# Kernel tuning notes

Measured on AMD Instinct MI355X. Metric: run time of the kernel, lower is better.

Reference implementation:

```python
import jax, jax.numpy as jnp
import numpy as np

DIM_MODEL = 1024
NUM_HEADS = 16
DIM_HEAD = 64
B, S = 2, 2048


def setup_inputs() -> dict:
    key = jax.random.key(0)
    ks = jax.random.split(key, 10)
    scale = 1.0 / np.sqrt(DIM_MODEL)
    inp = {
        "x": jax.random.normal(ks[0], (B, S, DIM_MODEL), dtype=jnp.float32),
        "padding_mask": jax.random.randint(ks[1], (B, S), 0, 2, dtype=jnp.int32),
        "Wq": jax.random.normal(ks[2], (DIM_MODEL, DIM_MODEL), dtype=jnp.float32) * scale,
        "bq": jnp.zeros((DIM_MODEL,), dtype=jnp.float32),
        "Wk": jax.random.normal(ks[3], (DIM_MODEL, DIM_MODEL), dtype=jnp.float32) * scale,
        "bk": jnp.zeros((DIM_MODEL,), dtype=jnp.float32),
        "Wv": jax.random.normal(ks[4], (DIM_MODEL, DIM_MODEL), dtype=jnp.float32) * scale,
        "bv": jnp.zeros((DIM_MODEL,), dtype=jnp.float32),
        "Wo": jax.random.normal(ks[5], (DIM_MODEL, DIM_MODEL), dtype=jnp.float32) * scale,
        "bo": jnp.zeros((DIM_MODEL,), dtype=jnp.float32),
    }
    return inp


def reference(x, padding_mask, Wq, bq, Wk, bk, Wv, bv, Wo, bo):
    b, s, _ = x.shape
    dot_scale = jnp.sqrt(jnp.asarray(DIM_HEAD, dtype=x.dtype))
    # projections -> (b, h, s, d)
    q = (x @ Wq + bq).reshape(b, s, NUM_HEADS, DIM_HEAD).transpose(0, 2, 1, 3)
    k = (x @ Wk + bk).reshape(b, s, NUM_HEADS, DIM_HEAD).transpose(0, 2, 1, 3)
    v = (x @ Wv + bv).reshape(b, s, NUM_HEADS, DIM_HEAD).transpose(0, 2, 1, 3)
    # scores (b, h, s, s)
    scores = jnp.einsum("bhqd,bhkd->bhqk", q, k) / dot_scale
    mask = (padding_mask == 1)[:, None, None, :]  # (b,1,1,s) over key positions
    scores = jnp.where(mask, -jnp.inf, scores)
    attn = jax.nn.softmax(scores, axis=-1)
    out = jnp.einsum("bhqk,bhkd->bhqd", attn, v)
    out = out.transpose(0, 2, 1, 3).reshape(b, s, NUM_HEADS * DIM_HEAD)
    return out @ Wo + bo
```

## Files before the change

### kernel.cpp

```cpp
#include <hip/hip_runtime.h>
#include <hip/hip_bf16.h>
#include <stdint.h>
#include <math.h>

#define D_MODEL 1024
#define NHEAD   16
#define DHEAD   64
#define BATCH   2
#define SEQ     2048
#define M_TOK   (BATCH * SEQ)

#define QSCALE 0.18033688011112042f

typedef __attribute__((ext_vector_type(8))) short   short8;
typedef __attribute__((ext_vector_type(8))) __bf16  bf16x8;
typedef __attribute__((ext_vector_type(4))) float   f32x4;

__device__ inline short f2bf(float f) {
  unsigned int u = __builtin_bit_cast(unsigned int, f);
  unsigned int r = (u + 0x7FFFu + ((u >> 16) & 1u)) >> 16;
  return (short)(unsigned short)r;
}
__device__ inline short f2bf_fast(float f) {
  unsigned int u = __builtin_bit_cast(unsigned int, f);
  return (short)(unsigned short)((u + 0x8000u) >> 16);
}

__device__ inline void gl_lds16(const void* g, void* l) {
  __builtin_amdgcn_global_load_lds((__attribute__((address_space(1))) void*)(g),
                                   (__attribute__((address_space(3))) void*)(l),
                                   16, 0, 0);
}

__device__ inline bf16x8 lds_frag(const short* p) {
  return *(const bf16x8*)(p);
}
__device__ inline bf16x8 lds_frag64(const short* p) {
  union { bf16x8 v; short4 h[2]; } u;
  u.h[0] = *(const short4*)(p);
  u.h[1] = *(const short4*)(p + 4);
  return u.v;
}

__global__ __launch_bounds__(256) void cvt_bf16(const float* __restrict__ in,
                                                short* __restrict__ out, int n4) {
  int i = blockIdx.x * 256 + threadIdx.x;
  if (i >= n4) return;
  f32x4 v = *(const f32x4*)(in + (size_t)i * 4);
  short4 o;
  o.x = f2bf(v[0]); o.y = f2bf(v[1]); o.z = f2bf(v[2]); o.w = f2bf(v[3]);
  *(short4*)(out + (size_t)i * 4) = o;
}

__global__ __launch_bounds__(256) void transpose_w(const float* __restrict__ w0,
                                                   const float* __restrict__ w1,
                                                   const float* __restrict__ w2,
                                                   const float* __restrict__ w3,
                                                   short* __restrict__ out) {
  __shared__ short tile[64][72];
  const float* W = blockIdx.z == 0 ? w0 : blockIdx.z == 1 ? w1 : blockIdx.z == 2 ? w2 : w3;
  short* O = out + (size_t)blockIdx.z * (D_MODEL * (size_t)D_MODEL);
  int n0 = blockIdx.x * 64, k0 = blockIdx.y * 64;
  int t = threadIdx.x;
#pragma unroll
  for (int i = 0; i < 16; ++i) {
    int idx = t + 256 * i;
    int r = idx >> 6, c = idx & 63;
    tile[r][c] = f2bf(W[(size_t)(k0 + r) * D_MODEL + n0 + c]);
  }
  __syncthreads();
#pragma unroll
  for (int i = 0; i < 16; ++i) {
    int idx = t + 256 * i;
    int r = idx >> 6, c = idx & 63;
    O[(size_t)(n0 + r) * D_MODEL + k0 + c] = tile[c][r];
  }
}

template <bool OUTF32, bool VT>
__global__ __launch_bounds__(256) void gemm128(const short* __restrict__ A,
                                               const short* __restrict__ Bt_base,
                                               const float* __restrict__ b0,
                                               const float* __restrict__ b1,
                                               const float* __restrict__ b2,
                                               void* __restrict__ out_base,
                                               short* __restrict__ vt,
                                               const int* __restrict__ pm) {
  const int z = blockIdx.z;
  const short* Bt   = Bt_base + (size_t)z * (D_MODEL * (size_t)D_MODEL);
  const float* bias = (z == 0) ? b0 : (z == 1) ? b1 : b2;

  __shared__ short As[128 * 64];
  __shared__ short Bs[128 * 64];

  const int t = threadIdx.x;
  const int lane = t & 63;
  const int wid = t >> 6;
  const int wm = (wid >> 1) * 64, wn = (wid & 1) * 64;
  const int m0 = blockIdx.x * 128, n0 = blockIdx.y * 128;
  const int cl = lane & 15, q = lane >> 4;
  const int sw = cl & 7;

  f32x4 acc[4][4];
#pragma unroll
  for (int i = 0; i < 4; ++i)
#pragma unroll
    for (int j = 0; j < 4; ++j) acc[i][j] = 0.0f;

  for (int k0 = 0; k0 < D_MODEL; k0 += 64) {
    __syncthreads();
#pragma unroll
    for (int i = 0; i < 4; ++i) {
      int c = t + 256 * i;
      int row = c >> 3;
      int cp  = c & 7;
      int col = ((cp ^ (row & 7)) * 8);
      gl_lds16(A  + (size_t)(m0 + row) * D_MODEL + k0 + col, (void*)(As + c * 8));
      gl_lds16(Bt + (size_t)(n0 + row) * D_MODEL + k0 + col, (void*)(Bs + c * 8));
    }
    __syncthreads();

    bf16x8 af[4][2], bfr[4][2];
#pragma unroll
    for (int mi = 0; mi < 4; ++mi) {
      af[mi][0] = lds_frag(As + (wm + mi * 16 + cl) * 64 + (q ^ sw) * 8);
      af[mi][1] = lds_frag(As + (wm + mi * 16 + cl) * 64 + ((4 + q) ^ sw) * 8);
    }
#pragma unroll
    for (int ni = 0; ni < 4; ++ni) {
      bfr[ni][0] = lds_frag(Bs + (wn + ni * 16 + cl) * 64 + (q ^ sw) * 8);
      bfr[ni][1] = lds_frag(Bs + (wn + ni * 16 + cl) * 64 + ((4 + q) ^ sw) * 8);
    }
#pragma unroll
    for (int mi = 0; mi < 4; ++mi)
#pragma unroll
      for (int ni = 0; ni < 4; ++ni) {
        acc[mi][ni] = __builtin_amdgcn_mfma_f32_16x16x32_bf16(af[mi][0], bfr[ni][0], acc[mi][ni], 0, 0, 0);
        acc[mi][ni] = __builtin_amdgcn_mfma_f32_16x16x32_bf16(af[mi][1], bfr[ni][1], acc[mi][ni], 0, 0, 0);
      }
  }

  const float oscale = (VT && z == 0) ? QSCALE : 1.0f;
  int4 mm[4];
  if (VT && z == 2) {
#pragma unroll
    for (int mi = 0; mi < 4; ++mi) {
      int rbase = m0 + wm + mi * 16 + q * 4;
      mm[mi] = *(const int4*)(pm + (size_t)(rbase >> 11) * SEQ + (rbase & (SEQ - 1)));
    }
  }
#pragma unroll
  for (int ni = 0; ni < 4; ++ni) {
    int col = n0 + wn + ni * 16 + cl;
    float bv = bias[col];
#pragma unroll
    for (int mi = 0; mi < 4; ++mi) {
      int rbase = m0 + wm + mi * 16 + q * 4;
      if (VT && z == 2) {
        short4 o4;
        o4.x = (mm[mi].x == 1) ? (short)0 : f2bf_fast(acc[mi][ni][0] + bv);
        o4.y = (mm[mi].y == 1) ? (short)0 : f2bf_fast(acc[mi][ni][1] + bv);
        o4.z = (mm[mi].z == 1) ? (short)0 : f2bf_fast(acc[mi][ni][2] + bv);
        o4.w = (mm[mi].w == 1) ? (short)0 : f2bf_fast(acc[mi][ni][3] + bv);
        int btok = rbase >> 11;
        int s    = rbase & (SEQ - 1);
        *(short4*)(vt + (size_t)btok * ((size_t)D_MODEL * SEQ) + (size_t)col * SEQ + s) = o4;
      } else {
#pragma unroll
        for (int r = 0; r < 4; ++r) {
          float v = (acc[mi][ni][r] + bv) * oscale;
          size_t idx = (size_t)(rbase + r) * D_MODEL + col;
          if (OUTF32) {
            ((float*)out_base)[idx] = v;
          } else {
            short* out = (short*)out_base + (size_t)z * ((size_t)M_TOK * D_MODEL);
            out[idx] = f2bf_fast(v);
          }
        }
      }
    }
  }
}

__global__ __launch_bounds__(256) void attn_flash(const short* __restrict__ Q,
                                                  const short* __restrict__ K,
                                                  const short* __restrict__ Vt,
                                                  const int*   __restrict__ mask,
                                                  short* __restrict__ ctx) {
  const int qb = blockIdx.x;
  const int h  = blockIdx.y;
  const int b  = blockIdx.z;

  __shared__ short QPs[8704];
  __shared__ short Ks[64 * 64];
  __shared__ short Vts[64 * 64];
  __shared__ short Us[64];

  const int t = threadIdx.x;
  const int lane = t & 63;
  const int wid = t >> 6;
  const int cl = lane & 15, q = lane >> 4;
  const int sw = cl & 7;

  const size_t rowQ0 = (size_t)b * SEQ + (size_t)qb * 128;
  const size_t rowK0 = (size_t)b * SEQ;
  const size_t vbase = ((size_t)b * D_MODEL + h * DHEAD) * SEQ;

#pragma unroll
  for (int i = 0; i < 4; ++i) {
    int c = t + 256 * i;
    int row = c >> 3, cp = c & 7;
    gl_lds16(Q + (rowQ0 + row) * D_MODEL + h * DHEAD + ((cp ^ (row & 7)) * 8),
             (void*)(QPs + c * 8));
  }
  __syncthreads();

  bf16x8 qf[2][2];
#pragma unroll
  for (int rb = 0; rb < 2; ++rb) {
    int row = wid * 32 + rb * 16 + cl;
    qf[rb][0] = lds_frag(QPs + row * 64 + (q ^ sw) * 8);
    qf[rb][1] = lds_frag(QPs + row * 64 + ((4 + q) ^ sw) * 8);
  }
  short* Psw = QPs + wid * (32 * 68);

  f32x4 lacc[2], oacc[2][4];
#pragma unroll
  for (int rb = 0; rb < 2; ++rb) {
    lacc[rb] = 0.0f;
#pragma unroll
    for (int dj = 0; dj < 4; ++dj) oacc[rb][dj] = 0.0f;
  }

  for (int kv0 = 0; kv0 < SEQ; kv0 += 64) {
    __syncthreads();

#pragma unroll
    for (int i = 0; i < 2; ++i) {
      int c = t + 256 * i;
      int row = c >> 3, cp = c & 7;
      gl_lds16(K + (rowK0 + kv0 + row) * D_MODEL + h * DHEAD + ((cp ^ (row & 7)) * 8),
               (void*)(Ks + c * 8));
      gl_lds16(Vt + vbase + (size_t)row * SEQ + kv0 + ((cp ^ (row & 7)) * 8),
               (void*)(Vts + c * 8));
    }
    if (t < 64) Us[t] = (mask[(size_t)b * SEQ + kv0 + t] == 1) ? (short)0 : (short)0x3F80;
    __syncthreads();

    f32x4 s[2][4];
#pragma unroll
    for (int j = 0; j < 4; ++j) {
      bf16x8 kf0 = lds_frag(Ks + (j * 16 + cl) * 64 + (q ^ sw) * 8);
      bf16x8 kf1 = lds_frag(Ks + (j * 16 + cl) * 64 + ((4 + q) ^ sw) * 8);
#pragma unroll
      for (int rb = 0; rb < 2; ++rb) {
        f32x4 sa = 0.0f;
        sa = __builtin_amdgcn_mfma_f32_16x16x32_bf16(qf[rb][0], kf0, sa, 0, 0, 0);
        sa = __builtin_amdgcn_mfma_f32_16x16x32_bf16(qf[rb][1], kf1, sa, 0, 0, 0);
        s[rb][j] = sa;
      }
    }

#pragma unroll
    for (int rb = 0; rb < 2; ++rb)
#pragma unroll
      for (int j = 0; j < 4; ++j)
#pragma unroll
        for (int r = 0; r < 4; ++r)
          Psw[(rb * 16 + q * 4 + r) * 68 + j * 16 + cl] = f2bf_fast(exp2f(s[rb][j][r]));

    asm volatile("" ::: "memory");

    bf16x8 pf[2][2];
#pragma unroll
    for (int rb = 0; rb < 2; ++rb) {
      pf[rb][0] = lds_frag64(Psw + (rb * 16 + cl) * 68 + q * 8);
      pf[rb][1] = lds_frag64(Psw + (rb * 16 + cl) * 68 + 32 + q * 8);
    }
    bf16x8 uf0 = lds_frag(Us + q * 8);
    bf16x8 uf1 = lds_frag(Us + 32 + q * 8);
#pragma unroll
    for (int dj = 0; dj < 4; ++dj) {
      bf16x8 vf0 = lds_frag(Vts + (dj * 16 + cl) * 64 + (q ^ sw) * 8);
      bf16x8 vf1 = lds_frag(Vts + (dj * 16 + cl) * 64 + ((4 + q) ^ sw) * 8);
#pragma unroll
      for (int rb = 0; rb < 2; ++rb) {
        oacc[rb][dj] = __builtin_amdgcn_mfma_f32_16x16x32_bf16(pf[rb][0], vf0, oacc[rb][dj], 0, 0, 0);
        oacc[rb][dj] = __builtin_amdgcn_mfma_f32_16x16x32_bf16(pf[rb][1], vf1, oacc[rb][dj], 0, 0, 0);
      }
    }
#pragma unroll
    for (int rb = 0; rb < 2; ++rb) {
      lacc[rb] = __builtin_amdgcn_mfma_f32_16x16x32_bf16(pf[rb][0], uf0, lacc[rb], 0, 0, 0);
      lacc[rb] = __builtin_amdgcn_mfma_f32_16x16x32_bf16(pf[rb][1], uf1, lacc[rb], 0, 0, 0);
    }
  }

#pragma unroll
  for (int rb = 0; rb < 2; ++rb)
#pragma unroll
    for (int dj = 0; dj < 4; ++dj)
#pragma unroll
      for (int r = 0; r < 4; ++r) {
        float lv = lacc[rb][r];
        float o = (lv > 0.0f) ? oacc[rb][dj][r] / lv : 0.0f;
        size_t row = rowQ0 + wid * 32 + rb * 16 + q * 4 + r;
        ctx[row * D_MODEL + h * DHEAD + dj * 16 + cl] = f2bf(o);
      }
}

extern "C" void kernel_launch(void* const* d_in, const int* in_sizes, int n_in,
                              void* d_out, int out_size, void* d_ws, size_t ws_size,
                              hipStream_t stream) {
  (void)in_sizes; (void)n_in; (void)out_size; (void)ws_size;

  const float* x  = (const float*)d_in[0];
  const int*   pm = (const int*)  d_in[1];
  const float* Wq = (const float*)d_in[2];
  const float* bq = (const float*)d_in[3];
  const float* Wk = (const float*)d_in[4];
  const float* bk = (const float*)d_in[5];
  const float* Wv = (const float*)d_in[6];
  const float* bv = (const float*)d_in[7];
  const float* Wo = (const float*)d_in[8];
  const float* bo = (const float*)d_in[9];

  const size_t WMAT = (size_t)D_MODEL * D_MODEL;
  const size_t TOKD = (size_t)M_TOK * D_MODEL;

  short* base = (short*)d_ws;
  short* Wt = base;
  short* xb = base + 4 * WMAT;
  short* Qw = xb + TOKD;
  short* Kw = Qw + TOKD;
  short* Vtw = Kw + TOKD;
  short* Cw = Vtw + TOKD;

  cvt_bf16<<<dim3((int)(TOKD / 4 / 256)), 256, 0, stream>>>(x, xb, (int)(TOKD / 4));
  transpose_w<<<dim3(16, 16, 4), 256, 0, stream>>>(Wq, Wk, Wv, Wo, Wt);
  gemm128<false, true><<<dim3(M_TOK / 128, D_MODEL / 128, 3), 256, 0, stream>>>(
      xb, Wt, bq, bk, bv, Qw, Vtw, pm);
  attn_flash<<<dim3(SEQ / 128, NHEAD, BATCH), 256, 0, stream>>>(Qw, Kw, Vtw, pm, Cw);
  gemm128<true, false><<<dim3(M_TOK / 128, D_MODEL / 128, 1), 256, 0, stream>>>(
      Cw, Wt + 3 * WMAT, bo, bo, bo, d_out, nullptr, nullptr);
}
```

Baseline: 230.1 us.

## Load attention K/V/Q fragments directly from global, precompute mask, narrow output GEMM tile

The attention kernel no longer stages Q, K and V^T through shared memory with block-wide barriers. Each wave now loads its MFMA fragments straight from global memory, which removes the per-iteration __syncthreads. The padding-mask bf16 vector is precomputed once inside the weight-transpose kernel. The output projection GEMM uses a 64-wide N tile to launch more blocks. The risk is that K/V tiles are now read redundantly by each of the four waves through cache instead of once per block, and the global loads are uncoalesced strided 16-byte reads.

Result: slower. 294.1 us (+27.8%).

```diff
diff --git a/kernel.cpp b/kernel.cpp
--- a/kernel.cpp
+++ b/kernel.cpp
@@ -33,6 +33,9 @@
 }
 
 __device__ inline bf16x8 lds_frag(const short* p) {
+  return *(const bf16x8*)(p);
+}
+__device__ inline bf16x8 g_frag(const short* p) {
   return *(const bf16x8*)(p);
 }
 __device__ inline bf16x8 lds_frag64(const short* p) {
@@ -56,12 +59,19 @@
                                                    const float* __restrict__ w1,
                                                    const float* __restrict__ w2,
                                                    const float* __restrict__ w3,
-                                                   short* __restrict__ out) {
+                                                   short* __restrict__ out,
+                                                   const int* __restrict__ pm,
+                                                   short* __restrict__ ubf) {
   __shared__ short tile[64][72];
   const float* W = blockIdx.z == 0 ? w0 : blockIdx.z == 1 ? w1 : blockIdx.z == 2 ? w2 : w3;
   short* O = out + (size_t)blockIdx.z * (D_MODEL * (size_t)D_MODEL);
   int n0 = blockIdx.x * 64, k0 = blockIdx.y * 64;
   int t = threadIdx.x;
+  if (blockIdx.z == 3 && blockIdx.x == 0 && blockIdx.y == 0) {
+#pragma unroll
+    for (int i = 0; i < M_TOK / 256; ++i)
+      ubf[t + 256 * i] = (pm[t + 256 * i] == 1) ? (short)0 : (short)0x3F80;
+  }
 #pragma unroll
   for (int i = 0; i < 16; ++i) {
     int idx = t + 256 * i;
@@ -77,7 +87,7 @@
   }
 }
 
-template <bool OUTF32, bool VT>
+template <bool OUTF32, bool VT, int TN>
 __global__ __launch_bounds__(256) void gemm128(const short* __restrict__ A,
                                                const short* __restrict__ Bt_base,
                                                const float* __restrict__ b0,
@@ -86,55 +96,61 @@
                                                void* __restrict__ out_base,
                                                short* __restrict__ vt,
                                                const int* __restrict__ pm) {
+  constexpr int NI = TN / 32;
   const int z = blockIdx.z;
   const short* Bt   = Bt_base + (size_t)z * (D_MODEL * (size_t)D_MODEL);
   const float* bias = (z == 0) ? b0 : (z == 1) ? b1 : b2;
 
   __shared__ short As[128 * 64];
-  __shared__ short Bs[128 * 64];
+  __shared__ short Bs[TN * 64];
 
   const int t = threadIdx.x;
   const int lane = t & 63;
   const int wid = t >> 6;
-  const int wm = (wid >> 1) * 64, wn = (wid & 1) * 64;
-  const int m0 = blockIdx.x * 128, n0 = blockIdx.y * 128;
+  const int wm = (wid >> 1) * 64, wn = (wid & 1) * (TN / 2);
+  const int m0 = blockIdx.x * 128, n0 = blockIdx.y * TN;
   const int cl = lane & 15, q = lane >> 4;
   const int sw = cl & 7;
 
-  f32x4 acc[4][4];
+  f32x4 acc[4][NI];
 #pragma unroll
   for (int i = 0; i < 4; ++i)
 #pragma unroll
-    for (int j = 0; j < 4; ++j) acc[i][j] = 0.0f;
+    for (int j = 0; j < NI; ++j) acc[i][j] = 0.0f;
 
   for (int k0 = 0; k0 < D_MODEL; k0 += 64) {
     __syncthreads();
 #pragma unroll
     for (int i = 0; i < 4; ++i) {
       int c = t + 256 * i;
-      int row = c >> 3;
-      int cp  = c & 7;
+      int row = c >> 3, cp = c & 7;
       int col = ((cp ^ (row & 7)) * 8);
-      gl_lds16(A  + (size_t)(m0 + row) * D_MODEL + k0 + col, (void*)(As + c * 8));
+      gl_lds16(A + (size_t)(m0 + row) * D_MODEL + k0 + col, (void*)(As + c * 8));
+    }
+#pragma unroll
+    for (int i = 0; i < NI; ++i) {
+      int c = t + 256 * i;
+      int row = c >> 3, cp = c & 7;
+      int col = ((cp ^ (row & 7)) * 8);
       gl_lds16(Bt + (size_t)(n0 + row) * D_MODEL + k0 + col, (void*)(Bs + c * 8));
     }
     __syncthreads();
 
-    bf16x8 af[4][2], bfr[4][2];
+    bf16x8 af[4][2], bfr[NI][2];
 #pragma unroll
     for (int mi = 0; mi < 4; ++mi) {
       af[mi][0] = lds_frag(As + (wm + mi * 16 + cl) * 64 + (q ^ sw) * 8);
       af[mi][1] = lds_frag(As + (wm + mi * 16 + cl) * 64 + ((4 + q) ^ sw) * 8);
     }
 #pragma unroll
-    for (int ni = 0; ni < 4; ++ni) {
+    for (int ni = 0; ni < NI; ++ni) {
       bfr[ni][0] = lds_frag(Bs + (wn + ni * 16 + cl) * 64 + (q ^ sw) * 8);
       bfr[ni][1] = lds_frag(Bs + (wn + ni * 16 + cl) * 64 + ((4 + q) ^ sw) * 8);
     }
 #pragma unroll
     for (int mi = 0; mi < 4; ++mi)
 #pragma unroll
-      for (int ni = 0; ni < 4; ++ni) {
+      for (int ni = 0; ni < NI; ++ni) {
         acc[mi][ni] = __builtin_amdgcn_mfma_f32_16x16x32_bf16(af[mi][0], bfr[ni][0], acc[mi][ni], 0, 0, 0);
         acc[mi][ni] = __builtin_amdgcn_mfma_f32_16x16x32_bf16(af[mi][1], bfr[ni][1], acc[mi][ni], 0, 0, 0);
       }
@@ -150,7 +166,7 @@
     }
   }
 #pragma unroll
-  for (int ni = 0; ni < 4; ++ni) {
+  for (int ni = 0; ni < NI; ++ni) {
     int col = n0 + wn + ni * 16 + cl;
     float bv = bias[col];
 #pragma unroll
@@ -185,44 +201,33 @@
 __global__ __launch_bounds__(256) void attn_flash(const short* __restrict__ Q,
                                                   const short* __restrict__ K,
                                                   const short* __restrict__ Vt,
-                                                  const int*   __restrict__ mask,
+                                                  const short* __restrict__ ubf,
                                                   short* __restrict__ ctx) {
   const int qb = blockIdx.x;
   const int h  = blockIdx.y;
   const int b  = blockIdx.z;
 
-  __shared__ short QPs[8704];
-  __shared__ short Ks[64 * 64];
-  __shared__ short Vts[64 * 64];
-  __shared__ short Us[64];
+  __shared__ short Ps[4][32 * 68];
 
   const int t = threadIdx.x;
   const int lane = t & 63;
   const int wid = t >> 6;
   const int cl = lane & 15, q = lane >> 4;
-  const int sw = cl & 7;
 
   const size_t rowQ0 = (size_t)b * SEQ + (size_t)qb * 128;
   const size_t rowK0 = (size_t)b * SEQ;
-  const size_t vbase = ((size_t)b * D_MODEL + h * DHEAD) * SEQ;
-
-#pragma unroll
-  for (int i = 0; i < 4; ++i) {
-    int c = t + 256 * i;
-    int row = c >> 3, cp = c & 7;
-    gl_lds16(Q + (rowQ0 + row) * D_MODEL + h * DHEAD + ((cp ^ (row & 7)) * 8),
-             (void*)(QPs + c * 8));
-  }
-  __syncthreads();
+  const int    hd    = h * DHEAD;
+  const size_t vbase = ((size_t)b * D_MODEL + hd) * SEQ;
+  const short* up    = ubf + (size_t)b * SEQ;
 
   bf16x8 qf[2][2];
 #pragma unroll
   for (int rb = 0; rb < 2; ++rb) {
-    int row = wid * 32 + rb * 16 + cl;
-    qf[rb][0] = lds_frag(QPs + row * 64 + (q ^ sw) * 8);
-    qf[rb][1] = lds_frag(QPs + row * 64 + ((4 + q) ^ sw) * 8);
-  }
-  short* Psw = QPs + wid * (32 * 68);
+    const short* qp = Q + (rowQ0 + wid * 32 + rb * 16 + cl) * D_MODEL + hd;
+    qf[rb][0] = g_frag(qp + q * 8);
+    qf[rb][1] = g_frag(qp + 32 + q * 8);
+  }
+  short* Psw = Ps[wid];
 
   f32x4 lacc[2], oacc[2][4];
 #pragma unroll
@@ -233,25 +238,12 @@
   }
 
   for (int kv0 = 0; kv0 < SEQ; kv0 += 64) {
-    __syncthreads();
-
-#pragma unroll
-    for (int i = 0; i < 2; ++i) {
-      int c = t + 256 * i;
-      int row = c >> 3, cp = c & 7;
-      gl_lds16(K + (rowK0 + kv0 + row) * D_MODEL + h * DHEAD + ((cp ^ (row & 7)) * 8),
-               (void*)(Ks + c * 8));
-      gl_lds16(Vt + vbase + (size_t)row * SEQ + kv0 + ((cp ^ (row & 7)) * 8),
-               (void*)(Vts + c * 8));
-    }
-    if (t < 64) Us[t] = (mask[(size_t)b * SEQ + kv0 + t] == 1) ? (short)0 : (short)0x3F80;
-    __syncthreads();
-
     f32x4 s[2][4];
 #pragma unroll
     for (int j = 0; j < 4; ++j) {
-      bf16x8 kf0 = lds_frag(Ks + (j * 16 + cl) * 64 + (q ^ sw) * 8);
-      bf16x8 kf1 = lds_frag(Ks + (j * 16 + cl) * 64 + ((4 + q) ^ sw) * 8);
+      const short* kp = K + (rowK0 + kv0 + j * 16 + cl) * D_MODEL + hd;
+      bf16x8 kf0 = g_frag(kp + q * 8);
+      bf16x8 kf1 = g_frag(kp + 32 + q * 8);
 #pragma unroll
       for (int rb = 0; rb < 2; ++rb) {
         f32x4 sa = 0.0f;
@@ -277,12 +269,13 @@
       pf[rb][0] = lds_frag64(Psw + (rb * 16 + cl) * 68 + q * 8);
       pf[rb][1] = lds_frag64(Psw + (rb * 16 + cl) * 68 + 32 + q * 8);
     }
-    bf16x8 uf0 = lds_frag(Us + q * 8);
-    bf16x8 uf1 = lds_frag(Us + 32 + q * 8);
+    bf16x8 uf0 = g_frag(up + kv0 + q * 8);
+    bf16x8 uf1 = g_frag(up + kv0 + 32 + q * 8);
 #pragma unroll
     for (int dj = 0; dj < 4; ++dj) {
-      bf16x8 vf0 = lds_frag(Vts + (dj * 16 + cl) * 64 + (q ^ sw) * 8);
-      bf16x8 vf1 = lds_frag(Vts + (dj * 16 + cl) * 64 + ((4 + q) ^ sw) * 8);
+      const short* vp = Vt + vbase + (size_t)(dj * 16 + cl) * SEQ + kv0;
+      bf16x8 vf0 = g_frag(vp + q * 8);
+      bf16x8 vf1 = g_frag(vp + 32 + q * 8);
 #pragma unroll
       for (int rb = 0; rb < 2; ++rb) {
         oacc[rb][dj] = __builtin_amdgcn_mfma_f32_16x16x32_bf16(pf[rb][0], vf0, oacc[rb][dj], 0, 0, 0);
@@ -305,7 +298,7 @@
         float lv = lacc[rb][r];
         float o = (lv > 0.0f) ? oacc[rb][dj][r] / lv : 0.0f;
         size_t row = rowQ0 + wid * 32 + rb * 16 + q * 4 + r;
-        ctx[row * D_MODEL + h * DHEAD + dj * 16 + cl] = f2bf(o);
+        ctx[row * D_MODEL + hd + dj * 16 + cl] = f2bf(o);
       }
 }
 
@@ -335,12 +328,13 @@
   short* Kw = Qw + TOKD;
   short* Vtw = Kw + TOKD;
   short* Cw = Vtw + TOKD;
+  short* Ub = Cw + TOKD;
 
   cvt_bf16<<<dim3((int)(TOKD / 4 / 256)), 256, 0, stream>>>(x, xb, (int)(TOKD / 4));
-  transpose_w<<<dim3(16, 16, 4), 256, 0, stream>>>(Wq, Wk, Wv, Wo, Wt);
-  gemm128<false, true><<<dim3(M_TOK / 128, D_MODEL / 128, 3), 256, 0, stream>>>(
+  transpose_w<<<dim3(16, 16, 4), 256, 0, stream>>>(Wq, Wk, Wv, Wo, Wt, pm, Ub);
+  gemm128<false, true, 128><<<dim3(M_TOK / 128, D_MODEL / 128, 3), 256, 0, stream>>>(
       xb, Wt, bq, bk, bv, Qw, Vtw, pm);
-  attn_flash<<<dim3(SEQ / 128, NHEAD, BATCH), 256, 0, stream>>>(Qw, Kw, Vtw, pm, Cw);
-  gemm128<true, false><<<dim3(M_TOK / 128, D_MODEL / 128, 1), 256, 0, stream>>>(
+  attn_flash<<<dim3(SEQ / 128, NHEAD, BATCH), 256, 0, stream>>>(Qw, Kw, Vtw, Ub, Cw);
+  gemm128<true, false, 64><<<dim3(M_TOK / 128, D_MODEL / 64, 1), 256, 0, stream>>>(
       Cw, Wt + 3 * WMAT, bo, bo, bo, d_out, nullptr, nullptr);
 }
```

## Fuse QKV projections sharing the A tile and stage V-transpose through LDS

Applied to the files above, without the earlier changes.

The QKV GEMM now computes all three projections in one block over a 128x64 output tile. Each loaded activation tile is reused for Q, K and V, so x is read once instead of three times. V output is staged in shared memory and written transposed with 16-byte coalesced stores, replacing scattered short4 writes. The output GEMM uses 128x64 tiles for more blocks. In exchange the QKV kernel holds three accumulator sets and uses more LDS, which may lower occupancy.

Measured after the change: 232.7 us. Within noise of the previous version (+1.1%).

```diff
diff --git a/kernel.cpp b/kernel.cpp
--- a/kernel.cpp
+++ b/kernel.cpp
@@ -77,107 +77,197 @@
   }
 }
 
-template <bool OUTF32, bool VT>
-__global__ __launch_bounds__(256) void gemm128(const short* __restrict__ A,
-                                               const short* __restrict__ Bt_base,
-                                               const float* __restrict__ b0,
-                                               const float* __restrict__ b1,
-                                               const float* __restrict__ b2,
-                                               void* __restrict__ out_base,
-                                               short* __restrict__ vt,
-                                               const int* __restrict__ pm) {
-  const int z = blockIdx.z;
-  const short* Bt   = Bt_base + (size_t)z * (D_MODEL * (size_t)D_MODEL);
-  const float* bias = (z == 0) ? b0 : (z == 1) ? b1 : b2;
-
-  __shared__ short As[128 * 64];
-  __shared__ short Bs[128 * 64];
+__global__ __launch_bounds__(256) void gemm_qkv(const short* __restrict__ A,
+                                                const short* __restrict__ Wt,
+                                                const float* __restrict__ bq,
+                                                const float* __restrict__ bk,
+                                                const float* __restrict__ bv,
+                                                short* __restrict__ Qw,
+                                                short* __restrict__ Kw,
+                                                short* __restrict__ vt,
+                                                const int* __restrict__ pm) {
+  const size_t WMAT = (size_t)D_MODEL * D_MODEL;
+  __shared__ short sh[20480];
+  short* As = sh;
 
   const int t = threadIdx.x;
   const int lane = t & 63;
   const int wid = t >> 6;
-  const int wm = (wid >> 1) * 64, wn = (wid & 1) * 64;
-  const int m0 = blockIdx.x * 128, n0 = blockIdx.y * 128;
+  const int wm = (wid >> 1) * 64, wn = (wid & 1) * 32;
+  const int m0 = blockIdx.x * 128, n0 = blockIdx.y * 64;
   const int cl = lane & 15, q = lane >> 4;
   const int sw = cl & 7;
 
-  f32x4 acc[4][4];
-#pragma unroll
-  for (int i = 0; i < 4; ++i)
-#pragma unroll
-    for (int j = 0; j < 4; ++j) acc[i][j] = 0.0f;
+  f32x4 acc[3][4][2];
+#pragma unroll
+  for (int z = 0; z < 3; ++z)
+#pragma unroll
+    for (int i = 0; i < 4; ++i)
+#pragma unroll
+      for (int j = 0; j < 2; ++j) acc[z][i][j] = 0.0f;
 
   for (int k0 = 0; k0 < D_MODEL; k0 += 64) {
     __syncthreads();
 #pragma unroll
     for (int i = 0; i < 4; ++i) {
       int c = t + 256 * i;
-      int row = c >> 3;
-      int cp  = c & 7;
+      int row = c >> 3, cp = c & 7;
       int col = ((cp ^ (row & 7)) * 8);
-      gl_lds16(A  + (size_t)(m0 + row) * D_MODEL + k0 + col, (void*)(As + c * 8));
-      gl_lds16(Bt + (size_t)(n0 + row) * D_MODEL + k0 + col, (void*)(Bs + c * 8));
-    }
-    __syncthreads();
-
-    bf16x8 af[4][2], bfr[4][2];
+      gl_lds16(A + (size_t)(m0 + row) * D_MODEL + k0 + col, (void*)(As + c * 8));
+    }
+#pragma unroll
+    for (int z = 0; z < 3; ++z)
+#pragma unroll
+      for (int i = 0; i < 2; ++i) {
+        int c = t + 256 * i;
+        int row = c >> 3, cp = c & 7;
+        int col = ((cp ^ (row & 7)) * 8);
+        gl_lds16(Wt + (size_t)z * WMAT + (size_t)(n0 + row) * D_MODEL + k0 + col,
+                 (void*)(sh + 8192 + z * 4096 + c * 8));
+      }
+    __syncthreads();
+
+    bf16x8 af[4][2];
 #pragma unroll
     for (int mi = 0; mi < 4; ++mi) {
       af[mi][0] = lds_frag(As + (wm + mi * 16 + cl) * 64 + (q ^ sw) * 8);
       af[mi][1] = lds_frag(As + (wm + mi * 16 + cl) * 64 + ((4 + q) ^ sw) * 8);
     }
 #pragma unroll
-    for (int ni = 0; ni < 4; ++ni) {
+    for (int z = 0; z < 3; ++z) {
+      const short* Bz = sh + 8192 + z * 4096;
+      bf16x8 bfr[2][2];
+#pragma unroll
+      for (int ni = 0; ni < 2; ++ni) {
+        bfr[ni][0] = lds_frag(Bz + (wn + ni * 16 + cl) * 64 + (q ^ sw) * 8);
+        bfr[ni][1] = lds_frag(Bz + (wn + ni * 16 + cl) * 64 + ((4 + q) ^ sw) * 8);
+      }
+#pragma unroll
+      for (int mi = 0; mi < 4; ++mi)
+#pragma unroll
+        for (int ni = 0; ni < 2; ++ni) {
+          acc[z][mi][ni] = __builtin_amdgcn_mfma_f32_16x16x32_bf16(af[mi][0], bfr[ni][0], acc[z][mi][ni], 0, 0, 0);
+          acc[z][mi][ni] = __builtin_amdgcn_mfma_f32_16x16x32_bf16(af[mi][1], bfr[ni][1], acc[z][mi][ni], 0, 0, 0);
+        }
+    }
+  }
+
+#pragma unroll
+  for (int ni = 0; ni < 2; ++ni) {
+    int col = n0 + wn + ni * 16 + cl;
+    float bqv = bq[col], bkv = bk[col];
+#pragma unroll
+    for (int mi = 0; mi < 4; ++mi) {
+      int rbase = m0 + wm + mi * 16 + q * 4;
+#pragma unroll
+      for (int r = 0; r < 4; ++r) {
+        size_t idx = (size_t)(rbase + r) * D_MODEL + col;
+        Qw[idx] = f2bf_fast((acc[0][mi][ni][r] + bqv) * QSCALE);
+        Kw[idx] = f2bf_fast(acc[1][mi][ni][r] + bkv);
+      }
+    }
+  }
+
+  __syncthreads();
+#pragma unroll
+  for (int ni = 0; ni < 2; ++ni) {
+    int cloc = wn + ni * 16 + cl;
+    float bvv = bv[n0 + cloc];
+#pragma unroll
+    for (int mi = 0; mi < 4; ++mi) {
+      int rbase = m0 + wm + mi * 16 + q * 4;
+      int4 mm = *(const int4*)(pm + (size_t)(rbase >> 11) * SEQ + (rbase & (SEQ - 1)));
+      short4 o4;
+      o4.x = (mm.x == 1) ? (short)0 : f2bf_fast(acc[2][mi][ni][0] + bvv);
+      o4.y = (mm.y == 1) ? (short)0 : f2bf_fast(acc[2][mi][ni][1] + bvv);
+      o4.z = (mm.z == 1) ? (short)0 : f2bf_fast(acc[2][mi][ni][2] + bvv);
+      o4.w = (mm.w == 1) ? (short)0 : f2bf_fast(acc[2][mi][ni][3] + bvv);
+      *(short4*)(sh + cloc * 136 + wm + mi * 16 + q * 4) = o4;
+    }
+  }
+  __syncthreads();
+  {
+    int cloc = t >> 2;
+    int soff = (t & 3) * 32;
+    int btok = m0 >> 11;
+    int sbase = m0 & (SEQ - 1);
+    short* vtp = vt + (size_t)btok * ((size_t)D_MODEL * SEQ) +
+                 (size_t)(n0 + cloc) * SEQ + sbase + soff;
+#pragma unroll
+    for (int k = 0; k < 4; ++k)
+      *(short8*)(vtp + k * 8) = *(const short8*)(sh + cloc * 136 + soff + k * 8);
+  }
+}
+
+__global__ __launch_bounds__(256) void gemm_out(const short* __restrict__ A,
+                                                const short* __restrict__ Bt,
+                                                const float* __restrict__ bias,
+                                                float* __restrict__ out) {
+  __shared__ short As[128 * 64];
+  __shared__ short Bs[64 * 64];
+
+  const int t = threadIdx.x;
+  const int lane = t & 63;
+  const int wid = t >> 6;
+  const int wm = (wid >> 1) * 64, wn = (wid & 1) * 32;
+  const int m0 = blockIdx.x * 128, n0 = blockIdx.y * 64;
+  const int cl = lane & 15, q = lane >> 4;
+  const int sw = cl & 7;
+
+  f32x4 acc[4][2];
+#pragma unroll
+  for (int i = 0; i < 4; ++i)
+#pragma unroll
+    for (int j = 0; j < 2; ++j) acc[i][j] = 0.0f;
+
+  for (int k0 = 0; k0 < D_MODEL; k0 += 64) {
+    __syncthreads();
+#pragma unroll
+    for (int i = 0; i < 4; ++i) {
+      int c = t + 256 * i;
+      int row = c >> 3, cp = c & 7;
+      int col = ((cp ^ (row & 7)) * 8);
+      gl_lds16(A + (size_t)(m0 + row) * D_MODEL + k0 + col, (void*)(As + c * 8));
+    }
+#pragma unroll
+    for (int i = 0; i < 2; ++i) {
+      int c = t + 256 * i;
+      int row = c >> 3, cp = c & 7;
+      int col = ((cp ^ (row & 7)) * 8);
+      gl_lds16(Bt + (size_t)(n0 + row) * D_MODEL + k0 + col, (void*)(Bs + c * 8));
+    }
+    __syncthreads();
+
+    bf16x8 af[4][2], bfr[2][2];
+#pragma unroll
+    for (int mi = 0; mi < 4; ++mi) {
+      af[mi][0] = lds_frag(As + (wm + mi * 16 + cl) * 64 + (q ^ sw) * 8);
+      af[mi][1] = lds_frag(As + (wm + mi * 16 + cl) * 64 + ((4 + q) ^ sw) * 8);
+    }
+#pragma unroll
+    for (int ni = 0; ni < 2; ++ni) {
       bfr[ni][0] = lds_frag(Bs + (wn + ni * 16 + cl) * 64 + (q ^ sw) * 8);
       bfr[ni][1] = lds_frag(Bs + (wn + ni * 16 + cl) * 64 + ((4 + q) ^ sw) * 8);
     }
 #pragma unroll
     for (int mi = 0; mi < 4; ++mi)
 #pragma unroll
-      for (int ni = 0; ni < 4; ++ni) {
+      for (int ni = 0; ni < 2; ++ni) {
         acc[mi][ni] = __builtin_amdgcn_mfma_f32_16x16x32_bf16(af[mi][0], bfr[ni][0], acc[mi][ni], 0, 0, 0);
         acc[mi][ni] = __builtin_amdgcn_mfma_f32_16x16x32_bf16(af[mi][1], bfr[ni][1], acc[mi][ni], 0, 0, 0);
       }
   }
 
-  const float oscale = (VT && z == 0) ? QSCALE : 1.0f;
-  int4 mm[4];
-  if (VT && z == 2) {
+#pragma unroll
+  for (int ni = 0; ni < 2; ++ni) {
+    int col = n0 + wn + ni * 16 + cl;
+    float bv = bias[col];
 #pragma unroll
     for (int mi = 0; mi < 4; ++mi) {
       int rbase = m0 + wm + mi * 16 + q * 4;
-      mm[mi] = *(const int4*)(pm + (size_t)(rbase >> 11) * SEQ + (rbase & (SEQ - 1)));
-    }
-  }
-#pragma unroll
-  for (int ni = 0; ni < 4; ++ni) {
-    int col = n0 + wn + ni * 16 + cl;
-    float bv = bias[col];
-#pragma unroll
-    for (int mi = 0; mi < 4; ++mi) {
-      int rbase = m0 + wm + mi * 16 + q * 4;
-      if (VT && z == 2) {
-        short4 o4;
-        o4.x = (mm[mi].x == 1) ? (short)0 : f2bf_fast(acc[mi][ni][0] + bv);
-        o4.y = (mm[mi].y == 1) ? (short)0 : f2bf_fast(acc[mi][ni][1] + bv);
-        o4.z = (mm[mi].z == 1) ? (short)0 : f2bf_fast(acc[mi][ni][2] + bv);
-        o4.w = (mm[mi].w == 1) ? (short)0 : f2bf_fast(acc[mi][ni][3] + bv);
-        int btok = rbase >> 11;
-        int s    = rbase & (SEQ - 1);
-        *(short4*)(vt + (size_t)btok * ((size_t)D_MODEL * SEQ) + (size_t)col * SEQ + s) = o4;
-      } else {
-#pragma unroll
-        for (int r = 0; r < 4; ++r) {
-          float v = (acc[mi][ni][r] + bv) * oscale;
-          size_t idx = (size_t)(rbase + r) * D_MODEL + col;
-          if (OUTF32) {
-            ((float*)out_base)[idx] = v;
-          } else {
-            short* out = (short*)out_base + (size_t)z * ((size_t)M_TOK * D_MODEL);
-            out[idx] = f2bf_fast(v);
-          }
-        }
-      }
+#pragma unroll
+      for (int r = 0; r < 4; ++r)
+        out[(size_t)(rbase + r) * D_MODEL + col] = acc[mi][ni][r] + bv;
     }
   }
 }
@@ -338,9 +428,9 @@
 
   cvt_bf16<<<dim3((int)(TOKD / 4 / 256)), 256, 0, stream>>>(x, xb, (int)(TOKD / 4));
   transpose_w<<<dim3(16, 16, 4), 256, 0, stream>>>(Wq, Wk, Wv, Wo, Wt);
-  gemm128<false, true><<<dim3(M_TOK / 128, D_MODEL / 128, 3), 256, 0, stream>>>(
-      xb, Wt, bq, bk, bv, Qw, Vtw, pm);
+  gemm_qkv<<<dim3(M_TOK / 128, D_MODEL / 64), 256, 0, stream>>>(
+      xb, Wt, bq, bk, bv, Qw, Kw, Vtw, pm);
   attn_flash<<<dim3(SEQ / 128, NHEAD, BATCH), 256, 0, stream>>>(Qw, Kw, Vtw, pm, Cw);
-  gemm128<true, false><<<dim3(M_TOK / 128, D_MODEL / 128, 1), 256, 0, stream>>>(
-      Cw, Wt + 3 * WMAT, bo, bo, bo, d_out, nullptr, nullptr);
-}
+  gemm_out<<<dim3(M_TOK / 128, D_MODEL / 64), 256, 0, stream>>>(
+      Cw, Wt + 3 * WMAT, bo, (float*)d_out);
+}
```
